# Kernel optimization log

Measured on AMD Instinct MI355X. Metric: run time of the kernel, lower is better.

The kernel has to match this reference:

```python
import jax, jax.numpy as jnp
import numpy as np

B, S, H = 1, 2048, 1024      # batch, seq, hidden_size
F = 4096                     # intermediate_size
E = 8                        # num_experts
K = 2                        # top-k routing


def setup_inputs() -> dict:
    key = jax.random.key(0)
    ks = jax.random.split(key, 7)
    s = 0.02  # init scale
    return {
        "x": jax.random.normal(ks[0], (B, S, H), jnp.float32),
        "gate_w": jax.random.normal(ks[1], (H, E), jnp.float32) * s,
        "gate_b": jnp.zeros((E,), jnp.float32),
        "w1": jax.random.normal(ks[2], (E, H, F), jnp.float32) * s,
        "b1": jnp.zeros((E, F), jnp.float32),
        "w2": jax.random.normal(ks[3], (E, F, H), jnp.float32) * s,
        "b2": jnp.zeros((E, H), jnp.float32),
    }


def reference(x, gate_w, gate_b, w1, b1, w2, b2):
    Bq, Sq, Hq = x.shape
    T = Bq * Sq
    xt = x.reshape(T, Hq)                              # [T,H] flatten tokens

    # --- router: softmax gate, top-k, renormalize top-k weights ---
    logits = xt @ gate_w + gate_b                      # [T,E]
    probs = jax.nn.softmax(logits, axis=-1)            # [T,E]
    top_v, top_i = jax.lax.top_k(probs, K)             # [T,K]
    top_v = top_v / jnp.sum(top_v, axis=-1, keepdims=True)
    combine = jnp.zeros((T, E), x.dtype).at[jnp.arange(T)[:, None], top_i].set(top_v)  # [T,E] sparse combine weights

    # --- experts: 2-layer FFN (ReLU), batched over experts ---
    h = jax.nn.relu(jnp.einsum('th,ehf->etf', xt, w1) + b1[:, None, :])   # [E,T,F]
    y = jnp.einsum('etf,efh->eth', h, w2) + b2[:, None, :]                # [E,T,H]

    # --- combine: weighted sum over selected experts (zeros elsewhere) ---
    out = jnp.einsum('te,eth->th', combine, y)          # [T,H]
    return out.reshape(Bq, Sq, Hq)
```

## Files before the change

### kernel.cpp

```cpp
#include <hip/hip_runtime.h>

#define TT 2048
#define HH 1024
#define FF 4096
#define EE 8
#define ROWS_CAP 5120

typedef __bf16 bf16;
typedef bf16 bf16x8 __attribute__((ext_vector_type(8)));
typedef bf16 bf16x4 __attribute__((ext_vector_type(4)));
typedef bf16 bf16x2 __attribute__((ext_vector_type(2)));
typedef float floatx4 __attribute__((ext_vector_type(4)));

#define OFF_W1T  ((size_t)0)
#define OFF_W2T  (OFF_W1T + (size_t)67108864)
#define OFF_XG   (OFF_W2T + (size_t)67108864)
#define OFF_H    (OFF_XG  + (size_t)10485760)
#define OFF_CNT  (OFF_H   + (size_t)41943040)
#define OFF_OFS  (OFF_CNT + (size_t)256)
#define OFF_TKE  (OFF_OFS + (size_t)256)
#define OFF_TKR  (OFF_TKE + (size_t)16384)
#define OFF_TKW  (OFF_TKR + (size_t)16384)
#define OFF_R2T  (OFF_TKW + (size_t)16384)
#define OFF_RW   (OFF_R2T + (size_t)20480)

__device__ __forceinline__ void gload16(const bf16* g, bf16* l) {
    __builtin_amdgcn_global_load_lds((const __attribute__((address_space(1))) void*)g,
                                     (__attribute__((address_space(3))) void*)l, 16, 0, 0);
}

__global__ __launch_bounds__(256) void transpose_cvt(const float* __restrict__ in,
                                                     bf16* __restrict__ out,
                                                     int R, int C) {
    __shared__ float tile[32][33];
    const int e  = blockIdx.z;
    const int r0 = blockIdx.y * 32, c0 = blockIdx.x * 32;
    const float* inp = in + (size_t)e * R * C;
    bf16* outp = out + (size_t)e * R * C;
    const int tid = threadIdx.x;
    {
        int r  = tid >> 3;
        int c4 = (tid & 7) << 2;
        floatx4 v = *(const floatx4*)&inp[(size_t)(r0 + r) * C + c0 + c4];
        tile[r][c4 + 0] = v[0]; tile[r][c4 + 1] = v[1];
        tile[r][c4 + 2] = v[2]; tile[r][c4 + 3] = v[3];
    }
    __syncthreads();
    {
        int rp = (tid & 15) << 1;
        int cl = tid >> 4;
#pragma unroll
        for (int p = 0; p < 2; ++p) {
            int c = cl + p * 16;
            bf16x2 v;
            v[0] = (bf16)tile[rp][c];
            v[1] = (bf16)tile[rp + 1][c];
            *(bf16x2*)&outp[(size_t)(c0 + c) * R + r0 + rp] = v;
        }
    }
}

__global__ __launch_bounds__(256) void router_kernel(const float* __restrict__ x,
                                                     const float* __restrict__ gw,
                                                     const float* __restrict__ gb,
                                                     int* __restrict__ counts,
                                                     int* __restrict__ tke,
                                                     int* __restrict__ tkr,
                                                     float* __restrict__ tkw) {
    const int wave = blockIdx.x * 4 + (threadIdx.x >> 6);
    const int lane = threadIdx.x & 63;
    const int nw = gridDim.x * 4;
    for (int t = wave; t < TT; t += nw) {
        const float* xr = x + (size_t)t * HH;
        double acc[EE];
#pragma unroll
        for (int e = 0; e < EE; ++e) acc[e] = 0.0;
        for (int h = lane; h < HH; h += 64) {
            double xv = (double)xr[h];
            const float* g = gw + (size_t)h * EE;
            floatx4 g0 = *(const floatx4*)&g[0];
            floatx4 g1 = *(const floatx4*)&g[4];
            acc[0] += xv * (double)g0[0]; acc[1] += xv * (double)g0[1];
            acc[2] += xv * (double)g0[2]; acc[3] += xv * (double)g0[3];
            acc[4] += xv * (double)g1[0]; acc[5] += xv * (double)g1[1];
            acc[6] += xv * (double)g1[2]; acc[7] += xv * (double)g1[3];
        }
#pragma unroll
        for (int e = 0; e < EE; ++e) {
            double v = acc[e];
            for (int s = 32; s > 0; s >>= 1) v += __shfl_xor(v, s, 64);
            acc[e] = v + (double)gb[e];
        }
        if (lane == 0) {
            int i1 = 0; double v1 = acc[0];
            for (int e = 1; e < EE; ++e) if (acc[e] > v1) { v1 = acc[e]; i1 = e; }
            int i2 = -1; double v2 = -1e300;
            for (int e = 0; e < EE; ++e) if (e != i1 && acc[e] > v2) { v2 = acc[e]; i2 = e; }
            double wa = 1.0 / (1.0 + exp(v2 - v1));
            double wb = 1.0 - wa;
            int r1 = atomicAdd(&counts[i1], 1);
            int r2 = atomicAdd(&counts[i2], 1);
            tke[t * 2 + 0] = i1; tke[t * 2 + 1] = i2;
            tkr[t * 2 + 0] = r1; tkr[t * 2 + 1] = r2;
            tkw[t * 2 + 0] = (float)wa; tkw[t * 2 + 1] = (float)wb;
        }
    }
}

__global__ void scan_offsets(const int* __restrict__ counts, int* __restrict__ offs) {
    if (threadIdx.x == 0 && blockIdx.x == 0) {
        int off = 0;
        for (int e = 0; e < EE; ++e) {
            offs[e] = off;
            off += (counts[e] + 127) & ~127;
        }
    }
}

__global__ __launch_bounds__(256) void gather_kernel(const float* __restrict__ x,
                                                     const int* __restrict__ tke,
                                                     const int* __restrict__ tkr,
                                                     const float* __restrict__ tkw,
                                                     const int* __restrict__ offs,
                                                     bf16* __restrict__ xg,
                                                     int* __restrict__ r2t,
                                                     float* __restrict__ rw) {
    const int pair = blockIdx.x;
    const int t = pair >> 1;
    const int e = tke[pair];
    const int row = offs[e] + tkr[pair];
    const float* xr = x + (size_t)t * HH;
    bf16* dst = xg + (size_t)row * HH;
    const int tid = threadIdx.x;
    floatx4 v = ((const floatx4*)xr)[tid];
    bf16x4 o;
    o[0] = (bf16)v[0]; o[1] = (bf16)v[1]; o[2] = (bf16)v[2]; o[3] = (bf16)v[3];
    ((bf16x4*)dst)[tid] = o;
    if (tid == 0) { r2t[row] = t; rw[row] = tkw[pair]; }
}

__global__ __launch_bounds__(256, 2) void gemm1_kernel(const bf16* __restrict__ A,
                                                       const bf16* __restrict__ Bt,
                                                       const float* __restrict__ b1,
                                                       bf16* __restrict__ Hout,
                                                       const int* __restrict__ counts,
                                                       const int* __restrict__ offs) {
    const int e = blockIdx.z, mt = blockIdx.y, nt = blockIdx.x;
    const int cnt = counts[e];
    if (mt * 128 >= cnt) return;
    const int row0 = offs[e] + mt * 128;
    const int K = HH;
    const bf16* Ab = A + (size_t)row0 * K;
    const bf16* Bb = Bt + ((size_t)e * FF + (size_t)nt * 128) * K;

    __shared__ bf16 As[128 * 32];
    __shared__ bf16 Bs[128 * 32];

    const int tid = threadIdx.x;
    const int lane = tid & 63, wave = tid >> 6;
    const int lrow = lane & 15, lq = lane >> 4;
    const int m_w = (wave & 1) << 6, n_w = (wave >> 1) << 6;
    const int swz = (lrow >> 1) & 3;
    const unsigned foff = (unsigned)((lq ^ swz) << 3);

    floatx4 acc[4][4];
#pragma unroll
    for (int i = 0; i < 4; ++i)
#pragma unroll
        for (int j = 0; j < 4; ++j) acc[i][j] = (floatx4){0.f, 0.f, 0.f, 0.f};

    const int c0 = tid, c1 = tid + 256;
    const int ar0 = c0 >> 2, ak0 = (c0 & 3) ^ ((ar0 >> 1) & 3);
    const int ar1 = c1 >> 2, ak1 = (c1 & 3) ^ ((ar1 >> 1) & 3);
    const unsigned lds0 = (unsigned)((tid & ~63) << 4);
    const unsigned lds1 = 4096u + lds0;
    const size_t ga0 = (size_t)ar0 * K + ak0 * 8;
    const size_t ga1 = (size_t)ar1 * K + ak1 * 8;

    for (int kt = 0; kt < K / 32; ++kt) {
        const int kb = kt * 32;
        gload16(Ab + ga0 + kb, (bf16*)((char*)As + lds0));
        gload16(Ab + ga1 + kb, (bf16*)((char*)As + lds1));
        gload16(Bb + ga0 + kb, (bf16*)((char*)Bs + lds0));
        gload16(Bb + ga1 + kb, (bf16*)((char*)Bs + lds1));
        asm volatile("s_waitcnt vmcnt(0)" ::: "memory");
        __syncthreads();

        bf16x8 af[4], bfr[4];
#pragma unroll
        for (int i = 0; i < 4; ++i) {
            int m = m_w + i * 16 + lrow;
            af[i] = *(const bf16x8*)&As[(unsigned)m * 32 + foff];
        }
#pragma unroll
        for (int j = 0; j < 4; ++j) {
            int n = n_w + j * 16 + lrow;
            bfr[j] = *(const bf16x8*)&Bs[(unsigned)n * 32 + foff];
        }
#pragma unroll
        for (int i = 0; i < 4; ++i)
#pragma unroll
            for (int j = 0; j < 4; ++j)
                acc[i][j] = __builtin_amdgcn_mfma_f32_16x16x32_bf16(af[i], bfr[j], acc[i][j], 0, 0, 0);
        __syncthreads();
    }

    const float* bias = b1 + (size_t)e * FF + (size_t)nt * 128;
    bf16* Hb = Hout + (size_t)row0 * FF + (size_t)nt * 128;
#pragma unroll
    for (int j = 0; j < 4; ++j) {
        int col = n_w + j * 16 + lrow;
        float bv = bias[col];
#pragma unroll
        for (int i = 0; i < 4; ++i)
#pragma unroll
            for (int r = 0; r < 4; ++r) {
                int mrow = m_w + i * 16 + (lq << 2) + r;
                float v = acc[i][j][r] + bv;
                Hb[(size_t)mrow * FF + col] = (bf16)(v > 0.f ? v : 0.f);
            }
    }
}

__global__ __launch_bounds__(256, 2) void gemm2_kernel(const bf16* __restrict__ Hin,
                                                       const bf16* __restrict__ Bt,
                                                       const float* __restrict__ b2,
                                                       float* __restrict__ out,
                                                       const int* __restrict__ counts,
                                                       const int* __restrict__ offs,
                                                       const int* __restrict__ r2t,
                                                       const float* __restrict__ rw) {
    const int e = blockIdx.z >> 1, ks = blockIdx.z & 1;
    const int mt = blockIdx.y, nt = blockIdx.x;
    const int cnt = counts[e];
    if (mt * 128 >= cnt) return;
    const int row0 = offs[e] + mt * 128;
    const int K = FF;
    const bf16* Ab = Hin + (size_t)row0 * K + ks * 2048;
    const bf16* Bb = Bt + ((size_t)e * HH + (size_t)nt * 128) * K + ks * 2048;

    __shared__ bf16 As[128 * 32];
    __shared__ bf16 Bs[128 * 32];

    const int tid = threadIdx.x;
    const int lane = tid & 63, wave = tid >> 6;
    const int lrow = lane & 15, lq = lane >> 4;
    const int m_w = (wave & 1) << 6, n_w = (wave >> 1) << 6;
    const int swz = (lrow >> 1) & 3;
    const unsigned foff = (unsigned)((lq ^ swz) << 3);

    floatx4 acc[4][4];
#pragma unroll
    for (int i = 0; i < 4; ++i)
#pragma unroll
        for (int j = 0; j < 4; ++j) acc[i][j] = (floatx4){0.f, 0.f, 0.f, 0.f};

    const int c0 = tid, c1 = tid + 256;
    const int ar0 = c0 >> 2, ak0 = (c0 & 3) ^ ((ar0 >> 1) & 3);
    const int ar1 = c1 >> 2, ak1 = (c1 & 3) ^ ((ar1 >> 1) & 3);
    const unsigned lds0 = (unsigned)((tid & ~63) << 4);
    const unsigned lds1 = 4096u + lds0;
    const size_t ga0 = (size_t)ar0 * K + ak0 * 8;
    const size_t ga1 = (size_t)ar1 * K + ak1 * 8;

    for (int kt = 0; kt < 64; ++kt) {
        const int kb = kt * 32;
        gload16(Ab + ga0 + kb, (bf16*)((char*)As + lds0));
        gload16(Ab + ga1 + kb, (bf16*)((char*)As + lds1));
        gload16(Bb + ga0 + kb, (bf16*)((char*)Bs + lds0));
        gload16(Bb + ga1 + kb, (bf16*)((char*)Bs + lds1));
        asm volatile("s_waitcnt vmcnt(0)" ::: "memory");
        __syncthreads();

        bf16x8 af[4], bfr[4];
#pragma unroll
        for (int i = 0; i < 4; ++i) {
            int m = m_w + i * 16 + lrow;
            af[i] = *(const bf16x8*)&As[(unsigned)m * 32 + foff];
        }
#pragma unroll
        for (int j = 0; j < 4; ++j) {
            int n = n_w + j * 16 + lrow;
            bfr[j] = *(const bf16x8*)&Bs[(unsigned)n * 32 + foff];
        }
#pragma unroll
        for (int i = 0; i < 4; ++i)
#pragma unroll
            for (int j = 0; j < 4; ++j)
                acc[i][j] = __builtin_amdgcn_mfma_f32_16x16x32_bf16(af[i], bfr[j], acc[i][j], 0, 0, 0);
        __syncthreads();
    }

    const float* bias = b2 + (size_t)e * HH + (size_t)nt * 128;
    const int valid = cnt - mt * 128;
#pragma unroll
    for (int i = 0; i < 4; ++i)
#pragma unroll
        for (int r = 0; r < 4; ++r) {
            int mrow = m_w + i * 16 + (lq << 2) + r;
            if (mrow < valid) {
                int row = row0 + mrow;
                int t = r2t[row];
                float w = rw[row];
                float* orow = out + (size_t)t * HH + (size_t)nt * 128;
#pragma unroll
                for (int j = 0; j < 4; ++j) {
                    int col = n_w + j * 16 + lrow;
                    float v = acc[i][j][r];
                    if (ks == 0) v += bias[col];
                    atomicAdd(&orow[col], w * v);
                }
            }
        }
}

extern "C" void kernel_launch(void* const* d_in, const int* in_sizes, int n_in,
                              void* d_out, int out_size, void* d_ws, size_t ws_size,
                              hipStream_t stream) {
    const float* x  = (const float*)d_in[0];
    const float* gw = (const float*)d_in[1];
    const float* gb = (const float*)d_in[2];
    const float* w1 = (const float*)d_in[3];
    const float* b1 = (const float*)d_in[4];
    const float* w2 = (const float*)d_in[5];
    const float* b2 = (const float*)d_in[6];
    float* out = (float*)d_out;
    char* ws = (char*)d_ws;

    bf16*  w1t  = (bf16*)(ws + OFF_W1T);
    bf16*  w2t  = (bf16*)(ws + OFF_W2T);
    bf16*  xg   = (bf16*)(ws + OFF_XG);
    bf16*  hbuf = (bf16*)(ws + OFF_H);
    int*   cnts = (int*)(ws + OFF_CNT);
    int*   ofs  = (int*)(ws + OFF_OFS);
    int*   tke  = (int*)(ws + OFF_TKE);
    int*   tkr  = (int*)(ws + OFF_TKR);
    float* tkw  = (float*)(ws + OFF_TKW);
    int*   r2t  = (int*)(ws + OFF_R2T);
    float* rwp  = (float*)(ws + OFF_RW);

    hipMemsetAsync(cnts, 0, 256, stream);
    hipMemsetAsync(xg, 0, (size_t)ROWS_CAP * HH * sizeof(bf16), stream);
    hipMemsetAsync(out, 0, (size_t)out_size * sizeof(float), stream);

    transpose_cvt<<<dim3(FF / 32, HH / 32, EE), 256, 0, stream>>>(w1, w1t, HH, FF);
    transpose_cvt<<<dim3(HH / 32, FF / 32, EE), 256, 0, stream>>>(w2, w2t, FF, HH);
    router_kernel<<<128, 256, 0, stream>>>(x, gw, gb, cnts, tke, tkr, tkw);
    scan_offsets<<<1, 64, 0, stream>>>(cnts, ofs);
    gather_kernel<<<TT * 2, 256, 0, stream>>>(x, tke, tkr, tkw, ofs, xg, r2t, rwp);
    gemm1_kernel<<<dim3(FF / 128, 16, EE), 256, 0, stream>>>(xg, w1t, b1, hbuf, cnts, ofs);
    gemm2_kernel<<<dim3(HH / 128, 16, EE * 2), 256, 0, stream>>>(hbuf, w2t, b2, out, cnts, ofs, r2t, rwp);
}
```

Before: 563.7 us.

## Replace gemm2 atomics with split-K partial buffer and combine kernel; widen transpose tiles

The weight transpose now works on 64x64 tiles and writes 16-byte bf16x8 vectors instead of 4-byte pairs, aiming to improve coalescing of the dominant weight-conversion traffic. gemm2 is split four ways over K and writes bf16 partial outputs per expert row into a buffer that reuses the no-longer-needed w1t region. A new combine kernel sums the partials for each token's two experts and applies the routing weights. This removes the fp32 atomicAdd scatter and the output memset. The cost is an extra kernel, more partial-output traffic, and bf16 rounding of the partial sums.

```diff
diff --git a/kernel.cpp b/kernel.cpp
--- a/kernel.cpp
+++ b/kernel.cpp
@@ -5,6 +5,7 @@
 #define FF 4096
 #define EE 8
 #define ROWS_CAP 5120
+#define KSPLIT2 4
 
 typedef __bf16 bf16;
 typedef bf16 bf16x8 __attribute__((ext_vector_type(8)));
@@ -21,8 +22,8 @@
 #define OFF_TKE  (OFF_OFS + (size_t)256)
 #define OFF_TKR  (OFF_TKE + (size_t)16384)
 #define OFF_TKW  (OFF_TKR + (size_t)16384)
-#define OFF_R2T  (OFF_TKW + (size_t)16384)
-#define OFF_RW   (OFF_R2T + (size_t)20480)
+#define OFF_ROW  (OFF_TKW + (size_t)16384)
+#define OFF_Y    OFF_W1T
 
 __device__ __forceinline__ void gload16(const bf16* g, bf16* l) {
     __builtin_amdgcn_global_load_lds((const __attribute__((address_space(1))) void*)g,
@@ -32,30 +33,34 @@
 __global__ __launch_bounds__(256) void transpose_cvt(const float* __restrict__ in,
                                                      bf16* __restrict__ out,
                                                      int R, int C) {
-    __shared__ float tile[32][33];
+    __shared__ float tile[64][67];
     const int e  = blockIdx.z;
-    const int r0 = blockIdx.y * 32, c0 = blockIdx.x * 32;
+    const int r0 = blockIdx.y * 64, c0 = blockIdx.x * 64;
     const float* inp = in + (size_t)e * R * C;
     bf16* outp = out + (size_t)e * R * C;
-    const int tid = threadIdx.x;
+    const int t = threadIdx.x;
     {
-        int r  = tid >> 3;
-        int c4 = (tid & 7) << 2;
-        floatx4 v = *(const floatx4*)&inp[(size_t)(r0 + r) * C + c0 + c4];
-        tile[r][c4 + 0] = v[0]; tile[r][c4 + 1] = v[1];
-        tile[r][c4 + 2] = v[2]; tile[r][c4 + 3] = v[3];
+        const int lr = t >> 4;
+        const int lc = (t & 15) << 2;
+#pragma unroll
+        for (int i = 0; i < 4; ++i) {
+            int r = lr + i * 16;
+            floatx4 v = *(const floatx4*)&inp[(size_t)(r0 + r) * C + c0 + lc];
+            tile[r][lc + 0] = v[0]; tile[r][lc + 1] = v[1];
+            tile[r][lc + 2] = v[2]; tile[r][lc + 3] = v[3];
+        }
     }
     __syncthreads();
     {
-        int rp = (tid & 15) << 1;
-        int cl = tid >> 4;
-#pragma unroll
-        for (int p = 0; p < 2; ++p) {
-            int c = cl + p * 16;
-            bf16x2 v;
-            v[0] = (bf16)tile[rp][c];
-            v[1] = (bf16)tile[rp + 1][c];
-            *(bf16x2*)&outp[(size_t)(c0 + c) * R + r0 + rp] = v;
+        const int c  = t >> 3;
+        const int rq = (t & 7) << 3;
+#pragma unroll
+        for (int i = 0; i < 2; ++i) {
+            int cc = c + i * 32;
+            bf16x8 o;
+#pragma unroll
+            for (int k = 0; k < 8; ++k) o[k] = (bf16)tile[rq + k][cc];
+            *(bf16x8*)&outp[(size_t)(c0 + cc) * R + r0 + rq] = o;
         }
     }
 }
@@ -120,11 +125,9 @@
 __global__ __launch_bounds__(256) void gather_kernel(const float* __restrict__ x,
                                                      const int* __restrict__ tke,
                                                      const int* __restrict__ tkr,
-                                                     const float* __restrict__ tkw,
                                                      const int* __restrict__ offs,
                                                      bf16* __restrict__ xg,
-                                                     int* __restrict__ r2t,
-                                                     float* __restrict__ rw) {
+                                                     int* __restrict__ rowOf) {
     const int pair = blockIdx.x;
     const int t = pair >> 1;
     const int e = tke[pair];
@@ -136,7 +139,7 @@
     bf16x4 o;
     o[0] = (bf16)v[0]; o[1] = (bf16)v[1]; o[2] = (bf16)v[2]; o[3] = (bf16)v[3];
     ((bf16x4*)dst)[tid] = o;
-    if (tid == 0) { r2t[row] = t; rw[row] = tkw[pair]; }
+    if (tid == 0) rowOf[pair] = row;
 }
 
 __global__ __launch_bounds__(256, 2) void gemm1_kernel(const bf16* __restrict__ A,
@@ -225,19 +228,18 @@
 __global__ __launch_bounds__(256, 2) void gemm2_kernel(const bf16* __restrict__ Hin,
                                                        const bf16* __restrict__ Bt,
                                                        const float* __restrict__ b2,
-                                                       float* __restrict__ out,
+                                                       bf16* __restrict__ Y,
                                                        const int* __restrict__ counts,
-                                                       const int* __restrict__ offs,
-                                                       const int* __restrict__ r2t,
-                                                       const float* __restrict__ rw) {
-    const int e = blockIdx.z >> 1, ks = blockIdx.z & 1;
+                                                       const int* __restrict__ offs) {
+    const int e = blockIdx.z >> 2, ks = blockIdx.z & 3;
     const int mt = blockIdx.y, nt = blockIdx.x;
     const int cnt = counts[e];
     if (mt * 128 >= cnt) return;
     const int row0 = offs[e] + mt * 128;
     const int K = FF;
-    const bf16* Ab = Hin + (size_t)row0 * K + ks * 2048;
-    const bf16* Bb = Bt + ((size_t)e * HH + (size_t)nt * 128) * K + ks * 2048;
+    const int KC = FF / KSPLIT2;
+    const bf16* Ab = Hin + (size_t)row0 * K + ks * KC;
+    const bf16* Bb = Bt + ((size_t)e * HH + (size_t)nt * 128) * K + ks * KC;
 
     __shared__ bf16 As[128 * 32];
     __shared__ bf16 Bs[128 * 32];
@@ -263,7 +265,7 @@
     const size_t ga0 = (size_t)ar0 * K + ak0 * 8;
     const size_t ga1 = (size_t)ar1 * K + ak1 * 8;
 
-    for (int kt = 0; kt < 64; ++kt) {
+    for (int kt = 0; kt < KC / 32; ++kt) {
         const int kb = kt * 32;
         gload16(Ab + ga0 + kb, (bf16*)((char*)As + lds0));
         gload16(Ab + ga1 + kb, (bf16*)((char*)As + lds1));
@@ -292,26 +294,40 @@
     }
 
     const float* bias = b2 + (size_t)e * HH + (size_t)nt * 128;
-    const int valid = cnt - mt * 128;
-#pragma unroll
-    for (int i = 0; i < 4; ++i)
-#pragma unroll
-        for (int r = 0; r < 4; ++r) {
-            int mrow = m_w + i * 16 + (lq << 2) + r;
-            if (mrow < valid) {
-                int row = row0 + mrow;
-                int t = r2t[row];
-                float w = rw[row];
-                float* orow = out + (size_t)t * HH + (size_t)nt * 128;
-#pragma unroll
-                for (int j = 0; j < 4; ++j) {
-                    int col = n_w + j * 16 + lrow;
-                    float v = acc[i][j][r];
-                    if (ks == 0) v += bias[col];
-                    atomicAdd(&orow[col], w * v);
-                }
+    bf16* Yb = Y + ((size_t)ks * ROWS_CAP + row0) * HH + (size_t)nt * 128;
+#pragma unroll
+    for (int j = 0; j < 4; ++j) {
+        int col = n_w + j * 16 + lrow;
+        float bv = (ks == 0) ? bias[col] : 0.f;
+#pragma unroll
+        for (int i = 0; i < 4; ++i)
+#pragma unroll
+            for (int r = 0; r < 4; ++r) {
+                int mrow = m_w + i * 16 + (lq << 2) + r;
+                Yb[(size_t)mrow * HH + col] = (bf16)(acc[i][j][r] + bv);
             }
-        }
+    }
+}
+
+__global__ __launch_bounds__(256) void combine_kernel(const bf16* __restrict__ Y,
+                                                      const int* __restrict__ rowOf,
+                                                      const float* __restrict__ tkw,
+                                                      float* __restrict__ out) {
+    const int t = blockIdx.x;
+    const int tid = threadIdx.x;
+    const int ra = rowOf[t * 2 + 0], rb = rowOf[t * 2 + 1];
+    const float wa = tkw[t * 2 + 0], wb = tkw[t * 2 + 1];
+    const int c = tid * 4;
+    float acc[4] = {0.f, 0.f, 0.f, 0.f};
+#pragma unroll
+    for (int ks = 0; ks < KSPLIT2; ++ks) {
+        bf16x4 a = *(const bf16x4*)&Y[((size_t)ks * ROWS_CAP + ra) * HH + c];
+        bf16x4 b = *(const bf16x4*)&Y[((size_t)ks * ROWS_CAP + rb) * HH + c];
+#pragma unroll
+        for (int k = 0; k < 4; ++k) acc[k] += wa * (float)a[k] + wb * (float)b[k];
+    }
+    floatx4 o; o[0] = acc[0]; o[1] = acc[1]; o[2] = acc[2]; o[3] = acc[3];
+    *(floatx4*)&out[(size_t)t * HH + c] = o;
 }
 
 extern "C" void kernel_launch(void* const* d_in, const int* in_sizes, int n_in,
@@ -331,23 +347,23 @@
     bf16*  w2t  = (bf16*)(ws + OFF_W2T);
     bf16*  xg   = (bf16*)(ws + OFF_XG);
     bf16*  hbuf = (bf16*)(ws + OFF_H);
+    bf16*  ybuf = (bf16*)(ws + OFF_Y);
     int*   cnts = (int*)(ws + OFF_CNT);
     int*   ofs  = (int*)(ws + OFF_OFS);
     int*   tke  = (int*)(ws + OFF_TKE);
     int*   tkr  = (int*)(ws + OFF_TKR);
     float* tkw  = (float*)(ws + OFF_TKW);
-    int*   r2t  = (int*)(ws + OFF_R2T);
-    float* rwp  = (float*)(ws + OFF_RW);
+    int*   rowOf= (int*)(ws + OFF_ROW);
 
     hipMemsetAsync(cnts, 0, 256, stream);
     hipMemsetAsync(xg, 0, (size_t)ROWS_CAP * HH * sizeof(bf16), stream);
-    hipMemsetAsync(out, 0, (size_t)out_size * sizeof(float), stream);
-
-    transpose_cvt<<<dim3(FF / 32, HH / 32, EE), 256, 0, stream>>>(w1, w1t, HH, FF);
-    transpose_cvt<<<dim3(HH / 32, FF / 32, EE), 256, 0, stream>>>(w2, w2t, FF, HH);
+
+    transpose_cvt<<<dim3(FF / 64, HH / 64, EE), 256, 0, stream>>>(w1, w1t, HH, FF);
+    transpose_cvt<<<dim3(HH / 64, FF / 64, EE), 256, 0, stream>>>(w2, w2t, FF, HH);
     router_kernel<<<128, 256, 0, stream>>>(x, gw, gb, cnts, tke, tkr, tkw);
     scan_offsets<<<1, 64, 0, stream>>>(cnts, ofs);
-    gather_kernel<<<TT * 2, 256, 0, stream>>>(x, tke, tkr, tkw, ofs, xg, r2t, rwp);
+    gather_kernel<<<TT * 2, 256, 0, stream>>>(x, tke, tkr, ofs, xg, rowOf);
     gemm1_kernel<<<dim3(FF / 128, 16, EE), 256, 0, stream>>>(xg, w1t, b1, hbuf, cnts, ofs);
-    gemm2_kernel<<<dim3(HH / 128, 16, EE * 2), 256, 0, stream>>>(hbuf, w2t, b2, out, cnts, ofs, r2t, rwp);
-}
+    gemm2_kernel<<<dim3(HH / 128, 16, EE * KSPLIT2), 256, 0, stream>>>(hbuf, w2t, b2, ybuf, cnts, ofs);
+    combine_kernel<<<TT, 256, 0, stream>>>(ybuf, rowOf, tkw, out);
+}
```

Result: faster. 532.2 us (-5.6%).
